# Performance work log

Measured on AMD Instinct MI355X. Metric: run time of the kernel, lower is better.

## Reference

```python
import jax, jax.numpy as jnp
from jax import lax
import numpy as np

DIM = 256
RES = 32          # D = H = W
HEADS = 8
HD = DIM // HEADS
SPLIT = 8
H_SP, W_SP = RES, SPLIT   # idx = 0: full-height stripe windows
SCALE = HD ** -0.5
B = 2
L = RES ** 3


def setup_inputs() -> dict:
    key = jax.random.key(0)
    k1, k2, k3 = jax.random.split(key, 3)
    qkv = jax.random.normal(k1, (3, B, L, DIM), dtype=jnp.float32)
    conv_w = jax.random.normal(k2, (DIM, 1, 3, 3), dtype=jnp.float32) * 0.1  # depthwise OIHW, groups=DIM
    conv_b = jax.random.normal(k3, (DIM,), dtype=jnp.float32) * 0.01
    return {"qkv": qkv, "conv_w": conv_w, "conv_b": conv_b}


def _to_window_imgs(x):
    # x: (B, L, C) -> per-depth-slice window images (Nw, C, H_sp, W_sp)
    Bc, Lc, C = x.shape
    nH, nW = RES // H_SP, RES // W_SP
    x = x.transpose(0, 2, 1).reshape(Bc, C, RES, nH, H_SP, nW, W_SP)      # B C D nH Hsp nW Wsp
    x = x.transpose(0, 2, 3, 5, 1, 4, 6)                                   # B D nH nW C Hsp Wsp
    return x.reshape(-1, C, H_SP, W_SP)


def _img_to_heads(xw):
    # (Nw, C, Hsp, Wsp) -> (Nw, heads, S, hd)
    return xw.reshape(-1, HEADS, HD, H_SP * W_SP).transpose(0, 1, 3, 2)


def reference(qkv, conv_w, conv_b):
    q, k, v = qkv[0], qkv[1], qkv[2]
    Bc, Lc, C = q.shape
    nH, nW = RES // H_SP, RES // W_SP

    qw = _img_to_heads(_to_window_imgs(q)) * SCALE    # (Nw, h, S, hd)
    kw = _img_to_heads(_to_window_imgs(k))
    vimg = _to_window_imgs(v)                          # (Nw, C, Hsp, Wsp)

    # LePE: depthwise 3x3 conv on v window images
    lepe = lax.conv_general_dilated(
        vimg, conv_w, window_strides=(1, 1), padding='SAME',
        feature_group_count=C,
        dimension_numbers=('NCHW', 'OIHW', 'NCHW')) + conv_b[None, :, None, None]
    lepe = _img_to_heads(lepe)                         # (Nw, h, S, hd)
    vw = _img_to_heads(vimg)

    attn = jax.nn.softmax(jnp.einsum('whsd,whtd->whst', qw, kw), axis=-1)
    x = jnp.einsum('whst,whtd->whsd', attn, vw) + lepe  # (Nw, h, S, hd)

    # windows -> image -> (B, L, C)
    x = x.transpose(0, 2, 1, 3).reshape(-1, H_SP * W_SP, C)               # (Nw, S, C)
    x = x.reshape(Bc, RES, nH, nW, H_SP, W_SP, C)
    x = x.transpose(0, 1, 2, 4, 3, 5, 6).reshape(Bc, RES, RES, RES, C)
    return x.reshape(Bc, -1, C)
```

## Files before the change

kernel.cpp:

```cpp
#include <hip/hip_runtime.h>
#include <stdint.h>


typedef short bf16x8 __attribute__((ext_vector_type(8)));
typedef uint16_t u16x4 __attribute__((ext_vector_type(4)));
typedef float f32x4 __attribute__((ext_vector_type(4)));
typedef uint32_t u32x2 __attribute__((ext_vector_type(2)));

#define KSTR 32
#define VSTR 264
#define PSTR 136

__device__ __forceinline__ float bf2f_lo(uint32_t u) {
    union { uint32_t i; float f; } x; x.i = u << 16; return x.f;
}
__device__ __forceinline__ float bf2f_hi(uint32_t u) {
    union { uint32_t i; float f; } x; x.i = u & 0xffff0000u; return x.f;
}
__device__ __forceinline__ uint16_t f2bf(float f) {
    union { float f; uint32_t i; } x; x.f = f;
    return (uint16_t)((x.i + 0x7fffu + ((x.i >> 16) & 1u)) >> 16);
}
__device__ __forceinline__ uint32_t fbits(float f) {
    union { float f; uint32_t i; } x; x.f = f; return x.i;
}

__global__ __launch_bounds__(256, 3)
void lepe_attn(const float* __restrict__ qkv,
               const float* __restrict__ conv_w,
               const float* __restrict__ conv_b,
               float* __restrict__ out)
{
    __shared__ uint16_t k_lds[256 * KSTR];
    __shared__ uint16_t vt_lds[32 * VSTR];
    __shared__ uint16_t p_lds[4 * 16 * PSTR];
    __shared__ float w_lds[288];
    __shared__ float b_lds[32];

    const int tid  = threadIdx.x;
    const int lane = tid & 63;
    const int wave = tid >> 6;
    const int l15  = lane & 15;
    const int quad = lane >> 4;

    const int blk  = blockIdx.x;
    const int head = blk & 7;
    const int wid  = blk >> 3;
    const int b    = wid >> 7;
    const int rem  = wid & 127;
    const int dpt  = rem >> 2;
    const int nw   = rem & 3;

    const long base_l = (long)dpt * 1024 + nw * 8;
    const int  hc     = head * 32;

    {
        const int  s = tid;
        const long l = base_l + (s >> 3) * 32 + (s & 7);
        const float* kp = qkv + (((long)(2 + b) * 32768 + l) * 256 + hc);
        const float* vp = qkv + (((long)(4 + b) * 32768 + l) * 256 + hc);
        #pragma unroll
        for (int j = 0; j < 8; ++j) {
            float4 kv = ((const float4*)kp)[j];
            u16x4 kb = { f2bf(kv.x), f2bf(kv.y), f2bf(kv.z), f2bf(kv.w) };
            *(u16x4*)&k_lds[s * KSTR + j * 4] = kb;
            float4 vv = ((const float4*)vp)[j];
            vt_lds[(j * 4 + 0) * VSTR + s] = f2bf(vv.x);
            vt_lds[(j * 4 + 1) * VSTR + s] = f2bf(vv.y);
            vt_lds[(j * 4 + 2) * VSTR + s] = f2bf(vv.z);
            vt_lds[(j * 4 + 3) * VSTR + s] = f2bf(vv.w);
        }
        for (int i = tid; i < 288; i += 256) w_lds[i] = conv_w[head * 288 + i];
        if (tid < 32) b_lds[tid] = conv_b[hc + tid];
    }
    __syncthreads();

    float wgt[18], bia[2];
    #pragma unroll
    for (int n = 0; n < 2; ++n) {
        #pragma unroll
        for (int i = 0; i < 9; ++i) wgt[n * 9 + i] = w_lds[(n * 16 + l15) * 9 + i];
        bia[n] = b_lds[n * 16 + l15];
    }

    const float c1 = 0.17677669529663687f * 1.4426950408889634f;
    const f32x4 zero4 = {0.f, 0.f, 0.f, 0.f};

    for (int it = 0; it < 4; ++it) {
        const int  rt   = wave * 4 + it;
        const int  sq   = rt * 16 + l15;
        const long ql   = base_l + (sq >> 3) * 32 + (sq & 7);
        const float* qp = qkv + (((long)b * 32768 + ql) * 256 + hc + quad * 8);
        float4 q0 = ((const float4*)qp)[0];
        float4 q1 = ((const float4*)qp)[1];
        bf16x8 qfrag;
        qfrag[0] = (short)f2bf(q0.x * c1); qfrag[1] = (short)f2bf(q0.y * c1);
        qfrag[2] = (short)f2bf(q0.z * c1); qfrag[3] = (short)f2bf(q0.w * c1);
        qfrag[4] = (short)f2bf(q1.x * c1); qfrag[5] = (short)f2bf(q1.y * c1);
        qfrag[6] = (short)f2bf(q1.z * c1); qfrag[7] = (short)f2bf(q1.w * c1);

        f32x4 accS[16];
        #pragma unroll
        for (int t = 0; t < 16; ++t) {
            bf16x8 afrag = *(const bf16x8*)&k_lds[(t * 16 + l15) * KSTR + quad * 8];
            accS[t] = __builtin_amdgcn_mfma_f32_16x16x32_bf16(afrag, qfrag, zero4, 0, 0, 0);
        }

        float ssum = 0.f;
        #pragma unroll
        for (int t = 0; t < 16; ++t) {
            #pragma unroll
            for (int r = 0; r < 4; ++r) {
                float p = exp2f(accS[t][r]);
                accS[t][r] = p;
                ssum += p;
            }
        }
        ssum += __shfl_xor(ssum, 16);
        ssum += __shfl_xor(ssum, 32);
        const float linv = __builtin_amdgcn_rcpf(ssum);
        float linv4[4];
        #pragma unroll
        for (int r = 0; r < 4; ++r) linv4[r] = __shfl(linv, quad * 4 + r);

        f32x4 accO[2] = {zero4, zero4};
        uint16_t* pw = &p_lds[wave * 16 * PSTR];
        #pragma unroll
        for (int half = 0; half < 2; ++half) {
            #pragma unroll
            for (int th = 0; th < 8; ++th) {
                const int t = half * 8 + th;
                uint32_t lo = ((fbits(accS[t][0]) + 0x8000u) >> 16)
                            | ((fbits(accS[t][1]) + 0x8000u) & 0xffff0000u);
                uint32_t hi = ((fbits(accS[t][2]) + 0x8000u) >> 16)
                            | ((fbits(accS[t][3]) + 0x8000u) & 0xffff0000u);
                u32x2 pk = {lo, hi};
                *(u32x2*)&pw[l15 * PSTR + th * 16 + quad * 4] = pk;
            }
            asm volatile("s_waitcnt lgkmcnt(0)" ::: "memory");
            #pragma unroll
            for (int c = 0; c < 4; ++c) {
                bf16x8 pa = *(const bf16x8*)&pw[l15 * PSTR + c * 32 + quad * 8];
                const int kb = half * 128 + c * 32 + quad * 8;
                bf16x8 vb0 = *(const bf16x8*)&vt_lds[l15 * VSTR + kb];
                accO[0] = __builtin_amdgcn_mfma_f32_16x16x32_bf16(pa, vb0, accO[0], 0, 0, 0);
                bf16x8 vb1 = *(const bf16x8*)&vt_lds[(16 + l15) * VSTR + kb];
                accO[1] = __builtin_amdgcn_mfma_f32_16x16x32_bf16(pa, vb1, accO[1], 0, 0, 0);
            }
            asm volatile("s_waitcnt lgkmcnt(0)" ::: "memory");
        }

        const int hrow = rt * 2 + (quad >> 1);
        const int wsel = quad & 1;
        #pragma unroll
        for (int n = 0; n < 2; ++n) {
            const int d = n * 16 + l15;
            float lep0 = bia[n], lep1 = bia[n], lep2 = bia[n], lep3 = bia[n];
            #pragma unroll
            for (int dy = 0; dy < 3; ++dy) {
                const int hh = hrow + dy - 1;
                float e0 = 0.f, e1 = 0.f, e2 = 0.f, e3 = 0.f, e4 = 0.f, e5 = 0.f;
                if (hh >= 0 && hh < 32) {
                    uint4 rv = *(const uint4*)&vt_lds[d * VSTR + hh * 8];
                    float c0 = bf2f_lo(rv.x), c1v = bf2f_hi(rv.x);
                    float c2 = bf2f_lo(rv.y), c3 = bf2f_hi(rv.y);
                    float c4 = bf2f_lo(rv.z), c5 = bf2f_hi(rv.z);
                    float c6 = bf2f_lo(rv.w), c7 = bf2f_hi(rv.w);
                    e0 = wsel ? c3 : 0.f;  e1 = wsel ? c4 : c0;
                    e2 = wsel ? c5 : c1v;  e3 = wsel ? c6 : c2;
                    e4 = wsel ? c7 : c3;   e5 = wsel ? 0.f : c4;
                }
                const float w0 = wgt[n * 9 + dy * 3 + 0];
                const float w1 = wgt[n * 9 + dy * 3 + 1];
                const float w2 = wgt[n * 9 + dy * 3 + 2];
                lep0 = fmaf(w0, e0, fmaf(w1, e1, fmaf(w2, e2, lep0)));
                lep1 = fmaf(w0, e1, fmaf(w1, e2, fmaf(w2, e3, lep1)));
                lep2 = fmaf(w0, e2, fmaf(w1, e3, fmaf(w2, e4, lep2)));
                lep3 = fmaf(w0, e3, fmaf(w1, e4, fmaf(w2, e5, lep3)));
            }
            const float lp[4] = {lep0, lep1, lep2, lep3};
            #pragma unroll
            for (int r = 0; r < 4; ++r) {
                const int s  = rt * 16 + quad * 4 + r;
                const int h  = s >> 3, w_ = s & 7;
                const float o = accO[n][r] * linv4[r] + lp[r];
                const long ol = base_l + h * 32 + w_;
                out[((long)b * 32768 + ol) * 256 + hc + d] = o;
            }
        }
    }
}

extern "C" void kernel_launch(void* const* d_in, const int* in_sizes, int n_in,
                              void* d_out, int out_size, void* d_ws, size_t ws_size,
                              hipStream_t stream)
{
    const float* qkv = (const float*)d_in[0];
    const float* cw  = (const float*)d_in[1];
    const float* cb  = (const float*)d_in[2];
    float* o = (float*)d_out;
    lepe_attn<<<2048, 256, 0, stream>>>(qkv, cw, cb, o);
}
```

Baseline: 333.7 us.

## Keep softmax probabilities in registers via permlane swaps instead of LDS round-trip

Replaces the per-wave P staging buffer in LDS with v_permlane32/16_swap register shuffles that rearrange the S accumulator layout directly into the A-operand layout for the PV MFMA. It also prefetches all Q fragments before the K/V load barrier, pads the K LDS stride to 40 to reduce bank conflicts, raises the occupancy target to 4 blocks per CU, and brackets the MFMA phases with s_setprio. This removes LDS writes, reads and waits from the inner loop and frees LDS for higher occupancy. The cost is more register pressure from the prefetched Q and packed P, which could spill under the tighter launch bound.

```diff
diff --git a/kernel.cpp b/kernel.cpp
--- a/kernel.cpp
+++ b/kernel.cpp
@@ -5,11 +5,10 @@
 typedef short bf16x8 __attribute__((ext_vector_type(8)));
 typedef uint16_t u16x4 __attribute__((ext_vector_type(4)));
 typedef float f32x4 __attribute__((ext_vector_type(4)));
-typedef uint32_t u32x2 __attribute__((ext_vector_type(2)));
-
-#define KSTR 32
+typedef uint32_t u32x4 __attribute__((ext_vector_type(4)));
+
+#define KSTR 40
 #define VSTR 264
-#define PSTR 136
 
 __device__ __forceinline__ float bf2f_lo(uint32_t u) {
     union { uint32_t i; float f; } x; x.i = u << 16; return x.f;
@@ -25,7 +24,7 @@
     union { float f; uint32_t i; } x; x.f = f; return x.i;
 }
 
-__global__ __launch_bounds__(256, 3)
+__global__ __launch_bounds__(256, 4)
 void lepe_attn(const float* __restrict__ qkv,
                const float* __restrict__ conv_w,
                const float* __restrict__ conv_b,
@@ -33,7 +32,6 @@
 {
     __shared__ uint16_t k_lds[256 * KSTR];
     __shared__ uint16_t vt_lds[32 * VSTR];
-    __shared__ uint16_t p_lds[4 * 16 * PSTR];
     __shared__ float w_lds[288];
     __shared__ float b_lds[32];
 
@@ -53,6 +51,18 @@
 
     const long base_l = (long)dpt * 1024 + nw * 8;
     const int  hc     = head * 32;
+
+    const float c1 = 0.17677669529663687f * 1.4426950408889634f;
+
+    float4 qpre[8];
+    #pragma unroll
+    for (int it = 0; it < 4; ++it) {
+        const int  sq = (wave * 4 + it) * 16 + l15;
+        const long ql = base_l + (sq >> 3) * 32 + (sq & 7);
+        const float* qp = qkv + (((long)b * 32768 + ql) * 256 + hc + quad * 8);
+        qpre[it * 2]     = ((const float4*)qp)[0];
+        qpre[it * 2 + 1] = ((const float4*)qp)[1];
+    }
 
     {
         const int  s = tid;
@@ -73,6 +83,18 @@
         for (int i = tid; i < 288; i += 256) w_lds[i] = conv_w[head * 288 + i];
         if (tid < 32) b_lds[tid] = conv_b[hc + tid];
     }
+
+    bf16x8 qfa[4];
+    #pragma unroll
+    for (int it = 0; it < 4; ++it) {
+        float4 q0 = qpre[it * 2], q1 = qpre[it * 2 + 1];
+        bf16x8 f;
+        f[0] = (short)f2bf(q0.x * c1); f[1] = (short)f2bf(q0.y * c1);
+        f[2] = (short)f2bf(q0.z * c1); f[3] = (short)f2bf(q0.w * c1);
+        f[4] = (short)f2bf(q1.x * c1); f[5] = (short)f2bf(q1.y * c1);
+        f[6] = (short)f2bf(q1.z * c1); f[7] = (short)f2bf(q1.w * c1);
+        qfa[it] = f;
+    }
     __syncthreads();
 
     float wgt[18], bia[2];
@@ -83,75 +105,24 @@
         bia[n] = b_lds[n * 16 + l15];
     }
 
-    const float c1 = 0.17677669529663687f * 1.4426950408889634f;
     const f32x4 zero4 = {0.f, 0.f, 0.f, 0.f};
 
+    #pragma unroll
     for (int it = 0; it < 4; ++it) {
-        const int  rt   = wave * 4 + it;
-        const int  sq   = rt * 16 + l15;
-        const long ql   = base_l + (sq >> 3) * 32 + (sq & 7);
-        const float* qp = qkv + (((long)b * 32768 + ql) * 256 + hc + quad * 8);
-        float4 q0 = ((const float4*)qp)[0];
-        float4 q1 = ((const float4*)qp)[1];
-        bf16x8 qfrag;
-        qfrag[0] = (short)f2bf(q0.x * c1); qfrag[1] = (short)f2bf(q0.y * c1);
-        qfrag[2] = (short)f2bf(q0.z * c1); qfrag[3] = (short)f2bf(q0.w * c1);
-        qfrag[4] = (short)f2bf(q1.x * c1); qfrag[5] = (short)f2bf(q1.y * c1);
-        qfrag[6] = (short)f2bf(q1.z * c1); qfrag[7] = (short)f2bf(q1.w * c1);
+        const int rt = wave * 4 + it;
 
         f32x4 accS[16];
+        __builtin_amdgcn_s_setprio(1);
         #pragma unroll
         for (int t = 0; t < 16; ++t) {
             bf16x8 afrag = *(const bf16x8*)&k_lds[(t * 16 + l15) * KSTR + quad * 8];
-            accS[t] = __builtin_amdgcn_mfma_f32_16x16x32_bf16(afrag, qfrag, zero4, 0, 0, 0);
-        }
-
-        float ssum = 0.f;
-        #pragma unroll
-        for (int t = 0; t < 16; ++t) {
-            #pragma unroll
-            for (int r = 0; r < 4; ++r) {
-                float p = exp2f(accS[t][r]);
-                accS[t][r] = p;
-                ssum += p;
-            }
-        }
-        ssum += __shfl_xor(ssum, 16);
-        ssum += __shfl_xor(ssum, 32);
-        const float linv = __builtin_amdgcn_rcpf(ssum);
-        float linv4[4];
-        #pragma unroll
-        for (int r = 0; r < 4; ++r) linv4[r] = __shfl(linv, quad * 4 + r);
-
-        f32x4 accO[2] = {zero4, zero4};
-        uint16_t* pw = &p_lds[wave * 16 * PSTR];
-        #pragma unroll
-        for (int half = 0; half < 2; ++half) {
-            #pragma unroll
-            for (int th = 0; th < 8; ++th) {
-                const int t = half * 8 + th;
-                uint32_t lo = ((fbits(accS[t][0]) + 0x8000u) >> 16)
-                            | ((fbits(accS[t][1]) + 0x8000u) & 0xffff0000u);
-                uint32_t hi = ((fbits(accS[t][2]) + 0x8000u) >> 16)
-                            | ((fbits(accS[t][3]) + 0x8000u) & 0xffff0000u);
-                u32x2 pk = {lo, hi};
-                *(u32x2*)&pw[l15 * PSTR + th * 16 + quad * 4] = pk;
-            }
-            asm volatile("s_waitcnt lgkmcnt(0)" ::: "memory");
-            #pragma unroll
-            for (int c = 0; c < 4; ++c) {
-                bf16x8 pa = *(const bf16x8*)&pw[l15 * PSTR + c * 32 + quad * 8];
-                const int kb = half * 128 + c * 32 + quad * 8;
-                bf16x8 vb0 = *(const bf16x8*)&vt_lds[l15 * VSTR + kb];
-                accO[0] = __builtin_amdgcn_mfma_f32_16x16x32_bf16(pa, vb0, accO[0], 0, 0, 0);
-                bf16x8 vb1 = *(const bf16x8*)&vt_lds[(16 + l15) * VSTR + kb];
-                accO[1] = __builtin_amdgcn_mfma_f32_16x16x32_bf16(pa, vb1, accO[1], 0, 0, 0);
-            }
-            asm volatile("s_waitcnt lgkmcnt(0)" ::: "memory");
-        }
+            accS[t] = __builtin_amdgcn_mfma_f32_16x16x32_bf16(afrag, qfa[it], zero4, 0, 0, 0);
+        }
+        __builtin_amdgcn_s_setprio(0);
 
         const int hrow = rt * 2 + (quad >> 1);
         const int wsel = quad & 1;
+        float lep[2][4];
         #pragma unroll
         for (int n = 0; n < 2; ++n) {
             const int d = n * 16 + l15;
@@ -178,14 +149,57 @@
                 lep2 = fmaf(w0, e2, fmaf(w1, e3, fmaf(w2, e4, lep2)));
                 lep3 = fmaf(w0, e3, fmaf(w1, e4, fmaf(w2, e5, lep3)));
             }
-            const float lp[4] = {lep0, lep1, lep2, lep3};
+            lep[n][0] = lep0; lep[n][1] = lep1; lep[n][2] = lep2; lep[n][3] = lep3;
+        }
+
+        uint32_t pkl[16], pkh[16];
+        float ssum = 0.f;
+        #pragma unroll
+        for (int t = 0; t < 16; ++t) {
+            float p0 = exp2f(accS[t][0]);
+            float p1 = exp2f(accS[t][1]);
+            float p2 = exp2f(accS[t][2]);
+            float p3 = exp2f(accS[t][3]);
+            ssum += (p0 + p1) + (p2 + p3);
+            pkl[t] = ((fbits(p0) + 0x8000u) >> 16) | ((fbits(p1) + 0x8000u) & 0xffff0000u);
+            pkh[t] = ((fbits(p2) + 0x8000u) >> 16) | ((fbits(p3) + 0x8000u) & 0xffff0000u);
+        }
+        ssum += __shfl_xor(ssum, 16);
+        ssum += __shfl_xor(ssum, 32);
+        const float linv = __builtin_amdgcn_rcpf(ssum);
+        float linv4[4];
+        #pragma unroll
+        for (int r = 0; r < 4; ++r) linv4[r] = __shfl(linv, quad * 4 + r);
+
+        f32x4 accO[2] = {zero4, zero4};
+        __builtin_amdgcn_s_setprio(1);
+        #pragma unroll
+        for (int cc = 0; cc < 8; ++cc) {
+            uint32_t a0 = pkl[2 * cc], a1 = pkl[2 * cc + 1];
+            uint32_t b0 = pkh[2 * cc], b1 = pkh[2 * cc + 1];
+            asm("v_permlane32_swap_b32 %0, %1" : "+v"(a0), "+v"(a1));
+            asm("v_permlane32_swap_b32 %0, %1" : "+v"(b0), "+v"(b1));
+            asm("v_permlane16_swap_b32 %0, %1" : "+v"(a0), "+v"(a1));
+            asm("v_permlane16_swap_b32 %0, %1" : "+v"(b0), "+v"(b1));
+            u32x4 pv = {a0, b0, a1, b1};
+            bf16x8 pa = __builtin_bit_cast(bf16x8, pv);
+            const int kb = cc * 32 + quad * 8;
+            bf16x8 vb0 = *(const bf16x8*)&vt_lds[l15 * VSTR + kb];
+            accO[0] = __builtin_amdgcn_mfma_f32_16x16x32_bf16(pa, vb0, accO[0], 0, 0, 0);
+            bf16x8 vb1 = *(const bf16x8*)&vt_lds[(16 + l15) * VSTR + kb];
+            accO[1] = __builtin_amdgcn_mfma_f32_16x16x32_bf16(pa, vb1, accO[1], 0, 0, 0);
+        }
+        __builtin_amdgcn_s_setprio(0);
+
+        #pragma unroll
+        for (int n = 0; n < 2; ++n) {
+            const int d = n * 16 + l15;
             #pragma unroll
             for (int r = 0; r < 4; ++r) {
                 const int s  = rt * 16 + quad * 4 + r;
                 const int h  = s >> 3, w_ = s & 7;
-                const float o = accO[n][r] * linv4[r] + lp[r];
                 const long ol = base_l + h * 32 + w_;
-                out[((long)b * 32768 + ol) * 256 + hc + d] = o;
+                out[((long)b * 32768 + ol) * 256 + hc + d] = accO[n][r] * linv4[r] + lep[n][r];
             }
         }
     }
```

New measurement: 394.5 us. +18.2%, slower.
